# Optimization experiments

Measured on AMD Instinct MI355X. Metric: run time of the kernel, lower is better.

Reference implementation:

```python
import jax, jax.numpy as jnp
import numpy as np

# ---- parameters (mirror torch module init) ----
DT = 1e-3            # clock_sim
T = 500              # tot_time / clock_sim
BS = 256             # trials_per_stimulus
N = 256              # neurons_n
# LIF (oscillator)
C_OSC = 1e-3; THR_OSC = 1.0; TAU_SYN = 5e-3; TAU_NEU = 1e-2
GAIN_SYN = 1e-3; VR_OSC = 0.0; REFR_OSC = 0.002 / DT
I_MIN = 0.12; I_STEP = 2e-4
# TDE
C_TDE = 1e-3; THR_TDE = 1.0; TAU_TRG = 1e-2; TAU_FAC = 5e-3
GAIN_FAC = 1.0; GAIN_TRG = 2.0; IFAC_THR = 0.1; BETA = 1e-2
VR_TDE = 0.0; REFR_TDE = 0.002 / DT
SCALE = 20.0  # SurrGradSpike.scale


@jax.custom_vjp
def spike(x):
    return (x > 0.0).astype(x.dtype)

def _spike_fwd(x):
    return spike(x), x

def _spike_bwd(x, g):
    return (g / (SCALE * jnp.abs(x) + 1.0) ** 2,)

spike.defvjp(_spike_fwd, _spike_bwd)


def setup_inputs() -> dict:
    key = jax.random.key(0)
    k1, _ = jax.random.split(key)
    # per-trial input spike train, (T, BS), Bernoulli(0.1)
    inp = (jax.random.uniform(k1, (T, BS)) < 0.1).astype(jnp.float32)
    # learnable current list (linspace as in sPLL.__init__)
    current_list = jnp.linspace(I_MIN, I_MIN + I_STEP * N, N, dtype=jnp.float32)
    return {"input": inp, "current_list": current_list}


def reference(input, current_list):
    steady = jnp.broadcast_to(current_list[None, :], (BS, N))  # LIF steady current

    def step(carry, inp_t):
        Vl, Il, crl, Vt, itrg, ifac, crt, spk_tde_prev = carry
        # expand per-trial input spike across all N neurons: (BS,) -> (BS, N)
        x = jnp.broadcast_to(inp_t[:, None], (BS, N))
        # ---- LIF step (driven by previous TDE spikes) ----
        Il = Il * (1.0 - DT / TAU_SYN) + GAIN_SYN * spk_tde_prev
        Vl = Vl + DT * (-Vl / TAU_NEU + (Il + steady) / C_OSC)
        spk_l = spike(Vl - THR_OSC)
        crl = REFR_OSC * spk_l + (1.0 - spk_l) * (crl - 1.0)
        Vl = (1.0 - spk_l) * Vl * (crl <= 0.0).astype(Vl.dtype) + spk_l * VR_OSC
        # ---- TDE step (trg = external input, fac = LIF spikes) ----
        ifac = spk_l * GAIN_FAC + ifac * (1.0 - spk_l)
        ifac = ifac * (1.0 - DT / TAU_FAC)
        itrg = itrg * (1.0 - DT / TAU_TRG)
        itrg = itrg + x * GAIN_TRG * ifac * (ifac > IFAC_THR).astype(ifac.dtype)
        Vt = Vt + DT * (-Vt / BETA + itrg / C_TDE)
        spk_t = spike(Vt - THR_TDE)
        crt = REFR_TDE * spk_t + (1.0 - spk_t) * (crt - 1.0)
        Vt = (1.0 - spk_t) * Vt * (crt <= 0.0).astype(Vt.dtype) + spk_t * VR_TDE
        return (Vl, Il, crl, Vt, itrg, ifac, crt, spk_t), (spk_l, spk_t)

    z = jnp.zeros((BS, N), dtype=jnp.float32)
    init = (jnp.ones((BS, N), dtype=jnp.float32), z, z,  # LIF: V=1, I=0, cr=0
            z, z, z, z,                                   # TDE: V, i_trg, i_fac, cr
            z)                                            # spikes_TDE_prev
    _, (spk_lif, spk_tde) = jax.lax.scan(step, init, input)
    return jnp.stack([spk_lif, spk_tde])  # (2, T, BS, N)
```

## Files before the change

kernel.cpp:

```cpp
#include <hip/hip_runtime.h>

static constexpr int T  = 500;
static constexpr int BS = 256;
static constexpr int N  = 256;
static constexpr int U  = 10;

#define FPBAR(x) asm("" : "+v"(x))

struct Cell { float Vl, Il, crl, Vt, itrg, ifac, crt; bool sp; };

__device__ __forceinline__ void do_step(float x, float steady, Cell& c,
                                        float& sl_out, float& st_out)
{
    const float RC = 999.99993896484375f;
    float u0 = c.Il * 0.8f;                      FPBAR(u0);
    float u1 = c.sp ? 1e-3f : 0.0f;
    c.Il = u0 + u1;                              FPBAR(c.Il);
    float u3 = -c.Vl * 100.0f;                   FPBAR(u3);
    float u4 = c.Il + steady;                    FPBAR(u4);
    float u6 = __builtin_fmaf(u4, RC, u3);       FPBAR(u6);
    c.Vl = __builtin_fmaf(1e-3f, u6, c.Vl);      FPBAR(c.Vl);
    bool  bl  = c.Vl > 1.0f;
    float crm = c.crl - 1.0f;
    bool  rg  = crm <= 0.0f;
    c.crl = bl ? 2.0f : crm;
    c.Vl  = (!bl && rg) ? c.Vl : 0.0f;
    sl_out = bl ? 1.0f : 0.0f;
    float u13 = bl ? 1.0f : c.ifac;
    c.ifac = u13 * 0.8f;                         FPBAR(c.ifac);
    float w0 = c.itrg * 0.9f;                    FPBAR(w0);
    float df  = c.ifac + c.ifac;
    float dfx = x * df;                          FPBAR(dfx);
    bool  m1  = c.ifac > 0.1f;
    float pulse = m1 ? dfx : 0.0f;
    c.itrg = w0 + pulse;                         FPBAR(c.itrg);
    float u18 = -c.Vt * 100.0f;                  FPBAR(u18);
    float u20 = __builtin_fmaf(c.itrg, RC, u18); FPBAR(u20);
    c.Vt = __builtin_fmaf(1e-3f, u20, c.Vt);     FPBAR(c.Vt);
    bool  bt  = c.Vt > 1.0f;
    float ctm = c.crt - 1.0f;
    bool  rg2 = ctm <= 0.0f;
    c.crt = bt ? 2.0f : ctm;
    c.Vt  = (!bt && rg2) ? c.Vt : 0.0f;
    st_out = bt ? 1.0f : 0.0f;
    c.sp = bt;
}

template <int PAR>
__device__ __forceinline__ void run_group(const float* sxp, float steady, Cell& c,
                                          float*& p0, float*& p1)
{
    const size_t step = (size_t)BS * N;
    const float2 x01 = *reinterpret_cast<const float2*>(sxp + 0);
    const float2 x23 = *reinterpret_cast<const float2*>(sxp + 2);
    const float2 x45 = *reinterpret_cast<const float2*>(sxp + 4);
    const float2 x67 = *reinterpret_cast<const float2*>(sxp + 6);
    const float2 x89 = *reinterpret_cast<const float2*>(sxp + 8);
    const float xs[U] = {x01.x, x01.y, x23.x, x23.y, x45.x,
                         x45.y, x67.x, x67.y, x89.x, x89.y};
    float sl, st;
#pragma unroll
    for (int j = 0; j < U; ++j) {
        do_step(xs[j], steady, c, sl, st);
        if ((j & 1) == PAR) {
            p0[(size_t)j * step] = sl;
            p1[(size_t)j * step] = st;
        }
    }
    p0 += (size_t)U * step;
    p1 += (size_t)U * step;
}

__global__ __launch_bounds__(256, 2) void spll_kernel(
    const float* __restrict__ inp,
    const float* __restrict__ current,
    float* __restrict__ out)
{
#pragma clang fp contract(off)
    const int b    = blockIdx.x & (BS - 1);
    const int role = blockIdx.x >> 8;
    const int n    = threadIdx.x;

    __shared__ __align__(16) float s_inp[T];
    for (int i = threadIdx.x; i < T; i += blockDim.x)
        s_inp[i] = inp[i * BS + b];
    __syncthreads();

    const float steady = current[n];
    Cell c = {1.0f, 0.0f, 0.0f, 0.0f, 0.0f, 0.0f, 0.0f, false};

    float* p0 = out + (size_t)b * N + n;
    float* p1 = p0 + (size_t)T * BS * N;

    if (role == 0) {
        for (int g = 0; g < T / U; ++g)
            run_group<0>(&s_inp[g * U], steady, c, p0, p1);
    } else {
        for (int g = 0; g < T / U; ++g)
            run_group<1>(&s_inp[g * U], steady, c, p0, p1);
    }
}

extern "C" void kernel_launch(void* const* d_in, const int* in_sizes, int n_in,
                              void* d_out, int out_size, void* d_ws, size_t ws_size,
                              hipStream_t stream) {
    const float* a0 = (const float*)d_in[0];
    const float* a1 = (const float*)d_in[1];
    const float* inp = a0;
    const float* cur = a1;
    if (n_in >= 2 && in_sizes[0] == N && in_sizes[1] == T * BS) { inp = a1; cur = a0; }
    float* out = (float*)d_out;
    spll_kernel<<<dim3(2 * BS), dim3(N), 0, stream>>>(inp, cur, out);
}
```

Measured before the change: 54.76 us.

## Process two neurons per thread with float2 stores and halve the grid

Each thread now simulates two adjacent neurons, interleaving their independent recurrences to expose ILP, and writes the spike pairs as float2 stores. Each block covers two trials, so the grid shrinks to 256 blocks and launch bounds drop to one block per SM. The goal is better instruction-level parallelism on the serial recurrence and wider stores. The trade-off is fewer waves resident to hide memory latency, and more registers per thread.

```diff
diff --git a/kernel.cpp b/kernel.cpp
--- a/kernel.cpp
+++ b/kernel.cpp
@@ -4,6 +4,7 @@
 static constexpr int BS = 256;
 static constexpr int N  = 256;
 static constexpr int U  = 10;
+static constexpr int LDP = 504;
 
 #define FPBAR(x) asm("" : "+v"(x))
 
@@ -47,10 +48,12 @@
 }
 
 template <int PAR>
-__device__ __forceinline__ void run_group(const float* sxp, float steady, Cell& c,
-                                          float*& p0, float*& p1)
+__device__ __forceinline__ void run_group(const float* sxp,
+                                          float st0, float st1,
+                                          Cell& c0, Cell& c1,
+                                          float2*& q0, float2*& q1)
 {
-    const size_t step = (size_t)BS * N;
+    const size_t step2 = (size_t)BS * N / 2;
     const float2 x01 = *reinterpret_cast<const float2*>(sxp + 0);
     const float2 x23 = *reinterpret_cast<const float2*>(sxp + 2);
     const float2 x45 = *reinterpret_cast<const float2*>(sxp + 4);
@@ -58,46 +61,57 @@
     const float2 x89 = *reinterpret_cast<const float2*>(sxp + 8);
     const float xs[U] = {x01.x, x01.y, x23.x, x23.y, x45.x,
                          x45.y, x67.x, x67.y, x89.x, x89.y};
-    float sl, st;
 #pragma unroll
     for (int j = 0; j < U; ++j) {
-        do_step(xs[j], steady, c, sl, st);
+        float sla, sta, slb, stb;
+        do_step(xs[j], st0, c0, sla, sta);
+        do_step(xs[j], st1, c1, slb, stb);
         if ((j & 1) == PAR) {
-            p0[(size_t)j * step] = sl;
-            p1[(size_t)j * step] = st;
+            q0[(size_t)j * step2] = make_float2(sla, slb);
+            q1[(size_t)j * step2] = make_float2(sta, stb);
         }
     }
-    p0 += (size_t)U * step;
-    p1 += (size_t)U * step;
+    q0 += (size_t)U * step2;
+    q1 += (size_t)U * step2;
 }
 
-__global__ __launch_bounds__(256, 2) void spll_kernel(
+__global__ __launch_bounds__(256, 1) void spll_kernel(
     const float* __restrict__ inp,
     const float* __restrict__ current,
     float* __restrict__ out)
 {
 #pragma clang fp contract(off)
-    const int b    = blockIdx.x & (BS - 1);
-    const int role = blockIdx.x >> 8;
-    const int n    = threadIdx.x;
+    const int B    = blockIdx.x & 127;
+    const int role = blockIdx.x >> 7;
+    const int half = threadIdx.x >> 7;
+    const int i    = threadIdx.x & 127;
+    const int b    = 2 * B + half;
+    const int n0   = 2 * i;
 
-    __shared__ __align__(16) float s_inp[T];
-    for (int i = threadIdx.x; i < T; i += blockDim.x)
-        s_inp[i] = inp[i * BS + b];
+    __shared__ __align__(16) float s_inp[2][LDP];
+    for (int t = threadIdx.x; t < T; t += blockDim.x) {
+        const float2 xv = *reinterpret_cast<const float2*>(&inp[t * BS + 2 * B]);
+        s_inp[0][t] = xv.x;
+        s_inp[1][t] = xv.y;
+    }
     __syncthreads();
 
-    const float steady = current[n];
-    Cell c = {1.0f, 0.0f, 0.0f, 0.0f, 0.0f, 0.0f, 0.0f, false};
+    const float2 stv = *reinterpret_cast<const float2*>(&current[n0]);
+    const float st0 = stv.x, st1 = stv.y;
 
-    float* p0 = out + (size_t)b * N + n;
-    float* p1 = p0 + (size_t)T * BS * N;
+    Cell c0 = {1.0f, 0.0f, 0.0f, 0.0f, 0.0f, 0.0f, 0.0f, false};
+    Cell c1 = {1.0f, 0.0f, 0.0f, 0.0f, 0.0f, 0.0f, 0.0f, false};
+
+    float2* q0 = reinterpret_cast<float2*>(out) + ((size_t)b * N + n0) / 2;
+    float2* q1 = q0 + (size_t)T * BS * N / 2;
+    const float* srow = s_inp[half];
 
     if (role == 0) {
         for (int g = 0; g < T / U; ++g)
-            run_group<0>(&s_inp[g * U], steady, c, p0, p1);
+            run_group<0>(&srow[g * U], st0, st1, c0, c1, q0, q1);
     } else {
         for (int g = 0; g < T / U; ++g)
-            run_group<1>(&s_inp[g * U], steady, c, p0, p1);
+            run_group<1>(&srow[g * U], st0, st1, c0, c1, q0, q1);
     }
 }
 
@@ -110,5 +124,5 @@
     const float* cur = a1;
     if (n_in >= 2 && in_sizes[0] == N && in_sizes[1] == T * BS) { inp = a1; cur = a0; }
     float* out = (float*)d_out;
-    spll_kernel<<<dim3(2 * BS), dim3(N), 0, stream>>>(inp, cur, out);
+    spll_kernel<<<dim3(2 * 128), dim3(256), 0, stream>>>(inp, cur, out);
 }
```

Result: slower. 73.40 us (+34.1%).

## Split output stores across three redundant block roles and branch on scalar input spike

Applied to the files above, without the earlier changes.

Each of three block roles recomputes the full recurrence and stores every third group of ten timesteps, instead of two roles storing alternating steps. This spreads the write traffic over more concurrent blocks, with occupancy hint raised to 3. The input spike value is made wave-uniform via readfirstlane, so the trigger-current update becomes a uniform branch that skips the multiply when the input is zero. The cost is 1.5x redundant compute. The branch relies on the input being exactly 0 or 1, since the multiply by x is dropped.

```diff
diff --git a/kernel.cpp b/kernel.cpp
--- a/kernel.cpp
+++ b/kernel.cpp
@@ -4,13 +4,14 @@
 static constexpr int BS = 256;
 static constexpr int N  = 256;
 static constexpr int U  = 10;
+static constexpr int R  = 3;
 
 #define FPBAR(x) asm("" : "+v"(x))
 
 struct Cell { float Vl, Il, crl, Vt, itrg, ifac, crt; bool sp; };
 
-__device__ __forceinline__ void do_step(float x, float steady, Cell& c,
-                                        float& sl_out, float& st_out)
+__device__ __forceinline__ void do_step(float x, unsigned xu, float steady,
+                                        Cell& c, float& sl_out, float& st_out)
 {
     const float RC = 999.99993896484375f;
     float u0 = c.Il * 0.8f;                      FPBAR(u0);
@@ -29,11 +30,15 @@
     float u13 = bl ? 1.0f : c.ifac;
     c.ifac = u13 * 0.8f;                         FPBAR(c.ifac);
     float w0 = c.itrg * 0.9f;                    FPBAR(w0);
-    float df  = c.ifac + c.ifac;
-    float dfx = x * df;                          FPBAR(dfx);
-    bool  m1  = c.ifac > 0.1f;
-    float pulse = m1 ? dfx : 0.0f;
-    c.itrg = w0 + pulse;                         FPBAR(c.itrg);
+    if (xu != 0u) {
+        float df    = c.ifac + c.ifac;
+        bool  m1    = c.ifac > 0.1f;
+        float pulse = m1 ? df : 0.0f;
+        float itn   = w0 + pulse;                FPBAR(itn);
+        c.itrg = itn;
+    } else {
+        c.itrg = w0;
+    }
     float u18 = -c.Vt * 100.0f;                  FPBAR(u18);
     float u20 = __builtin_fmaf(c.itrg, RC, u18); FPBAR(u20);
     c.Vt = __builtin_fmaf(1e-3f, u20, c.Vt);     FPBAR(c.Vt);
@@ -46,7 +51,7 @@
     c.sp = bt;
 }
 
-template <int PAR>
+template <bool STORE>
 __device__ __forceinline__ void run_group(const float* sxp, float steady, Cell& c,
                                           float*& p0, float*& p1)
 {
@@ -61,8 +66,9 @@
     float sl, st;
 #pragma unroll
     for (int j = 0; j < U; ++j) {
-        do_step(xs[j], steady, c, sl, st);
-        if ((j & 1) == PAR) {
+        unsigned xu = __builtin_amdgcn_readfirstlane(__float_as_uint(xs[j]));
+        do_step(xs[j], xu, steady, c, sl, st);
+        if (STORE) {
             p0[(size_t)j * step] = sl;
             p1[(size_t)j * step] = st;
         }
@@ -71,7 +77,7 @@
     p1 += (size_t)U * step;
 }
 
-__global__ __launch_bounds__(256, 2) void spll_kernel(
+__global__ __launch_bounds__(256, 3) void spll_kernel(
     const float* __restrict__ inp,
     const float* __restrict__ current,
     float* __restrict__ out)
@@ -92,12 +98,13 @@
     float* p0 = out + (size_t)b * N + n;
     float* p1 = p0 + (size_t)T * BS * N;
 
-    if (role == 0) {
-        for (int g = 0; g < T / U; ++g)
-            run_group<0>(&s_inp[g * U], steady, c, p0, p1);
-    } else {
-        for (int g = 0; g < T / U; ++g)
-            run_group<1>(&s_inp[g * U], steady, c, p0, p1);
+    int phase = role;
+    for (int g = 0; g < T / U; ++g) {
+        if (phase == 0)
+            run_group<true>(&s_inp[g * U], steady, c, p0, p1);
+        else
+            run_group<false>(&s_inp[g * U], steady, c, p0, p1);
+        phase = (phase == 2) ? 0 : (phase + 1);
     }
 }
 
@@ -110,5 +117,5 @@
     const float* cur = a1;
     if (n_in >= 2 && in_sizes[0] == N && in_sizes[1] == T * BS) { inp = a1; cur = a0; }
     float* out = (float*)d_out;
-    spll_kernel<<<dim3(2 * BS), dim3(N), 0, stream>>>(inp, cur, out);
+    spll_kernel<<<dim3(R * BS), dim3(N), 0, stream>>>(inp, cur, out);
 }
```

Result: slower. 70.47 us (+28.7%).

## Stage spikes in LDS and write alternate time groups with float4 stores

Applied to the files above, without the earlier changes.

Each of the two redundant blocks per trial now takes ownership of alternating 10-step groups instead of alternating time steps. The owning block buffers spike outputs in shared memory and then writes them out as coalesced float4 stores, in place of scattered per-step scalar stores. This is meant to cut the number of global store instructions and improve write efficiency. In exchange it adds two block barriers per owned group and extra LDS traffic, and the writes become burstier.

```diff
diff --git a/kernel.cpp b/kernel.cpp
--- a/kernel.cpp
+++ b/kernel.cpp
@@ -6,6 +6,12 @@
 static constexpr int U  = 10;
 
 #define FPBAR(x) asm("" : "+v"(x))
+#define LBAR()                                            \
+    do {                                                  \
+        asm volatile("s_waitcnt lgkmcnt(0)" ::: "memory");\
+        __builtin_amdgcn_s_barrier();                     \
+        __builtin_amdgcn_sched_barrier(0);                \
+    } while (0)
 
 struct Cell { float Vl, Il, crl, Vt, itrg, ifac, crt; bool sp; };
 
@@ -46,31 +52,6 @@
     c.sp = bt;
 }
 
-template <int PAR>
-__device__ __forceinline__ void run_group(const float* sxp, float steady, Cell& c,
-                                          float*& p0, float*& p1)
-{
-    const size_t step = (size_t)BS * N;
-    const float2 x01 = *reinterpret_cast<const float2*>(sxp + 0);
-    const float2 x23 = *reinterpret_cast<const float2*>(sxp + 2);
-    const float2 x45 = *reinterpret_cast<const float2*>(sxp + 4);
-    const float2 x67 = *reinterpret_cast<const float2*>(sxp + 6);
-    const float2 x89 = *reinterpret_cast<const float2*>(sxp + 8);
-    const float xs[U] = {x01.x, x01.y, x23.x, x23.y, x45.x,
-                         x45.y, x67.x, x67.y, x89.x, x89.y};
-    float sl, st;
-#pragma unroll
-    for (int j = 0; j < U; ++j) {
-        do_step(xs[j], steady, c, sl, st);
-        if ((j & 1) == PAR) {
-            p0[(size_t)j * step] = sl;
-            p1[(size_t)j * step] = st;
-        }
-    }
-    p0 += (size_t)U * step;
-    p1 += (size_t)U * step;
-}
-
 __global__ __launch_bounds__(256, 2) void spll_kernel(
     const float* __restrict__ inp,
     const float* __restrict__ current,
@@ -81,23 +62,52 @@
     const int role = blockIdx.x >> 8;
     const int n    = threadIdx.x;
 
-    __shared__ __align__(16) float s_inp[T];
+    __shared__ __align__(16) float s_inp[512];
+    __shared__ __align__(16) float s_spk[U * 2 * N];
     for (int i = threadIdx.x; i < T; i += blockDim.x)
         s_inp[i] = inp[i * BS + b];
     __syncthreads();
 
     const float steady = current[n];
     Cell c = {1.0f, 0.0f, 0.0f, 0.0f, 0.0f, 0.0f, 0.0f, false};
+    const size_t step = (size_t)BS * N;
 
-    float* p0 = out + (size_t)b * N + n;
-    float* p1 = p0 + (size_t)T * BS * N;
+    for (int g = 0; g < T / U; ++g) {
+        const float* sxp = &s_inp[g * U];
+        const float2 x01 = *reinterpret_cast<const float2*>(sxp + 0);
+        const float2 x23 = *reinterpret_cast<const float2*>(sxp + 2);
+        const float2 x45 = *reinterpret_cast<const float2*>(sxp + 4);
+        const float2 x67 = *reinterpret_cast<const float2*>(sxp + 6);
+        const float2 x89 = *reinterpret_cast<const float2*>(sxp + 8);
+        const float xs[U] = {x01.x, x01.y, x23.x, x23.y, x45.x,
+                             x45.y, x67.x, x67.y, x89.x, x89.y};
+        float sl, st;
 
-    if (role == 0) {
-        for (int g = 0; g < T / U; ++g)
-            run_group<0>(&s_inp[g * U], steady, c, p0, p1);
-    } else {
-        for (int g = 0; g < T / U; ++g)
-            run_group<1>(&s_inp[g * U], steady, c, p0, p1);
+        if ((g & 1) == role) {
+#pragma unroll
+            for (int j = 0; j < U; ++j) {
+                do_step(xs[j], steady, c, sl, st);
+                s_spk[j * (2 * N) + n]     = sl;
+                s_spk[j * (2 * N) + N + n] = st;
+            }
+            LBAR();
+#pragma unroll
+            for (int k = 0; k < 5; ++k) {
+                const int f0 = k * 1024 + threadIdx.x * 4;
+                const int j  = f0 >> 9;
+                const int s  = (f0 >> 8) & 1;
+                const int n0 = f0 & (N - 1);
+                const float4 v = *reinterpret_cast<const float4*>(&s_spk[f0]);
+                float* dst = out + ((size_t)s * T + (size_t)(g * U + j)) * step
+                                 + (size_t)b * N + n0;
+                *reinterpret_cast<float4*>(dst) = v;
+            }
+            LBAR();
+        } else {
+#pragma unroll
+            for (int j = 0; j < U; ++j)
+                do_step(xs[j], steady, c, sl, st);
+        }
     }
 }
 
```

After: 60.99 us. 11.4% more time.
